# Kernel tuning notes

Hardware: AMD Instinct MI355X
Metric: run time of the kernel (lower is better)

## Reference

```python
import jax, jax.numpy as jnp
import numpy as np

GAMMA = 20
LAMBDA_INV = 25.0


def setup_inputs() -> dict:
    key = jax.random.key(0)
    k1, k2 = jax.random.split(key)
    B, P, D = 128, 512, 384
    z = jax.random.normal(k1, (B, P, D), dtype=jnp.float32)
    view_ids = jax.random.randint(k2, (P,), 0, 2, dtype=jnp.int64)
    return {"z": z, "view_ids": view_ids}


def reference(z, view_ids):
    B, P, D = z.shape
    # [B, P, P] pairwise similarity per image
    sim = jnp.einsum('bpd,bqd->bpq', z, z)
    # valid pairs: different view and not self
    mask_view = view_ids[None, :] != view_ids[:, None]          # [P, P]
    mask = mask_view & ~jnp.eye(P, dtype=bool)
    sim = jnp.where(mask[None, :, :], sim, jnp.float32(-1.0))
    best_sim = sim.max(axis=2)                                   # [B, P]
    best_j = sim.argmax(axis=2)                                  # [B, P]
    # flatten across batch, global top-gamma anchors
    best_sim_flat = best_sim.reshape(-1)                         # [B*P]
    offsets = jnp.arange(B, dtype=best_j.dtype)[:, None] * P
    best_j_flat = (best_j + offsets).reshape(-1)                 # [B*P]
    topk_vals, topk_idx = jax.lax.top_k(best_sim_flat, GAMMA)
    z_flat = z.reshape(-1, D)
    z1 = z_flat[topk_idx]                                        # anchors
    z2 = z_flat[best_j_flat[topk_idx]]                           # matches
    loss = LAMBDA_INV * jnp.mean((z1 - z2) ** 2)
    fmatch_avg_cos = jax.lax.stop_gradient(topk_vals.mean())
    return loss, fmatch_avg_cos
```

## Files before the change

kernel.cpp:

```cpp
#include <hip/hip_runtime.h>


#define NB 128
#define NP 512
#define ND 384
#define NGAMMA 20
#define NKS 12

typedef __attribute__((ext_vector_type(8))) short short8;
typedef __attribute__((ext_vector_type(4))) float f32x4;

__device__ __forceinline__ unsigned short f2bf(float f) {
    unsigned int u = __float_as_uint(f);
    u += 0x7fffu + ((u >> 16) & 1u);
    return (unsigned short)(u >> 16);
}

__device__ __forceinline__ void gload16(const void* gptr, void* lptr) {
    __builtin_amdgcn_global_load_lds(
        (const __attribute__((address_space(1))) void*)gptr,
        (__attribute__((address_space(3))) void*)lptr, 16, 0, 0);
}

__global__ __launch_bounds__(256) void fm_convert(
    const float* __restrict__ z, unsigned short* __restrict__ zt)
{
    __shared__ float ls[128][36];

    const int tid  = threadIdx.x;
    const int bid  = blockIdx.x;
    const int b    = bid / (NKS * 4);
    const int rem  = bid % (NKS * 4);
    const int kt   = rem >> 2;
    const int pblk = rem & 3;

    const float* zsrc = z + ((size_t)b * NP + pblk * 128) * ND + kt * 32;
#pragma unroll
    for (int i = 0; i < 4; ++i) {
        const int f   = tid + i * 256;
        const int row = f >> 3, c4 = f & 7;
        *(float4*)&ls[row][c4 * 4] = *(const float4*)(zsrc + (size_t)row * ND + c4 * 4);
    }
    __syncthreads();

    const int kg = tid >> 6, lane = tid & 63;
    unsigned short* dst = zt + (((size_t)b * NKS + kt) * 4 + kg) * 4096
                             + (size_t)pblk * 1024;
#pragma unroll
    for (int it = 0; it < 2; ++it) {
        const int row = it * 64 + lane;
        const float4 v0 = *(const float4*)&ls[row][kg * 8];
        const float4 v1 = *(const float4*)&ls[row][kg * 8 + 4];
        short8 s;
        s[0] = (short)f2bf(v0.x); s[1] = (short)f2bf(v0.y);
        s[2] = (short)f2bf(v0.z); s[3] = (short)f2bf(v0.w);
        s[4] = (short)f2bf(v1.x); s[5] = (short)f2bf(v1.y);
        s[6] = (short)f2bf(v1.z); s[7] = (short)f2bf(v1.w);
        *(short8*)(dst + (size_t)row * 8) = s;
    }
}

__global__ __launch_bounds__(512, 4) void fm_gemm(
    const unsigned short* __restrict__ zt, const int* __restrict__ view,
    float* __restrict__ pval, int* __restrict__ pidx)
{
    __shared__ __align__(16) unsigned short Ah[3][4][128][8];
    __shared__ __align__(16) unsigned short Bh[3][4][128][8];
    __shared__ int vs[NP];
    float* lsv = (float*)&Ah[0][0][0][0];
    int*   lsi = (int*)lsv + 512;
    float* lqv = (float*)lsv + 1024;
    int*   lqi = (int*)lsv + 1280;

    const int tid  = threadIdx.x;
    const int lane = tid & 63;
    const int wid  = tid >> 6;
    const int wr   = wid >> 2;
    const int wc2  = wid & 3;
    const int g    = lane >> 4, r = lane & 15;

    const int bid  = blockIdx.x;
    const int gidx = (bid & 7) * 160 + (bid >> 3);
    const int b    = gidx / 10;
    const int t    = gidx % 10;
    int tr, tc;
    if (t < 4)      { tr = 0; tc = t; }
    else if (t < 7) { tr = 1; tc = t - 3; }
    else if (t < 9) { tr = 2; tc = t - 5; }
    else            { tr = 3; tc = 3; }
    const bool diag = (tr == tc);
    const int p0 = tr * 128, q0 = tc * 128;

    vs[tid] = view[tid];
    __builtin_amdgcn_sched_barrier(0);

    f32x4 acc[4][2];
#pragma unroll
    for (int mi = 0; mi < 4; ++mi)
#pragma unroll
        for (int ni = 0; ni < 2; ++ni) acc[mi][ni] = (f32x4){0.f, 0.f, 0.f, 0.f};

#define STAGE(BUF, KT)                                                           \
    do {                                                                         \
        const int kg_ = wid >> 1;                                                \
        const int rb_ = (wid & 1) * 64;                                          \
        const size_t pl_ = (((size_t)b * NKS + (KT)) * 4 + kg_) * 4096;          \
        gload16(zt + pl_ + (size_t)(p0 + rb_ + lane) * 8, &Ah[BUF][kg_][rb_][0]); \
        gload16(zt + pl_ + (size_t)(q0 + rb_ + lane) * 8, &Bh[BUF][kg_][rb_][0]); \
    } while (0)

#define COMPUTE(BUF)                                                             \
    do {                                                                         \
        short8 ah_[4], bh_[2];                                                   \
        _Pragma("unroll")                                                        \
        for (int mi = 0; mi < 4; ++mi)                                           \
            ah_[mi] = *(const short8*)&Ah[BUF][g][wr * 64 + mi * 16 + r][0];     \
        _Pragma("unroll")                                                        \
        for (int ni = 0; ni < 2; ++ni)                                           \
            bh_[ni] = *(const short8*)&Bh[BUF][g][wc2 * 32 + ni * 16 + r][0];    \
        _Pragma("unroll")                                                        \
        for (int mi = 0; mi < 4; ++mi)                                           \
            _Pragma("unroll")                                                    \
            for (int ni = 0; ni < 2; ++ni)                                       \
                acc[mi][ni] = __builtin_amdgcn_mfma_f32_16x16x32_bf16(           \
                    ah_[mi], bh_[ni], acc[mi][ni], 0, 0, 0);                     \
    } while (0)

    STAGE(0, 0);
    STAGE(1, 1);
#pragma unroll
    for (int kt = 0; kt < NKS; ++kt) {
        if (kt < NKS - 1) asm volatile("s_waitcnt vmcnt(2)" ::: "memory");
        else              asm volatile("s_waitcnt vmcnt(0)" ::: "memory");
        __builtin_amdgcn_s_barrier();
        __builtin_amdgcn_sched_barrier(0);
        if (kt + 2 < NKS) STAGE((kt + 2) % 3, kt + 2);
        __builtin_amdgcn_sched_barrier(0);
        COMPUTE(kt % 3);
    }
#undef STAGE
#undef COMPUTE

#pragma unroll
    for (int mi = 0; mi < 4; ++mi) {
#pragma unroll
        for (int j = 0; j < 4; ++j) {
            const int prow = p0 + wr * 64 + mi * 16 + g * 4 + j;
            const int rv = vs[prow];
            float bv = -2.0f; int bq = 0;
#pragma unroll
            for (int ni = 0; ni < 2; ++ni) {
                const int q = q0 + wc2 * 32 + ni * 16 + r;
                const float v = (vs[q] != rv) ? acc[mi][ni][j] : -1.0f;
                if (v > bv) { bv = v; bq = q; }
            }
#pragma unroll
            for (int off = 1; off < 16; off <<= 1) {
                const float ov = __shfl_xor(bv, off);
                const int   oq = __shfl_xor(bq, off);
                if (ov > bv || (ov == bv && oq < bq)) { bv = ov; bq = oq; }
            }
            if (r == 0) {
                lsv[(wr * 4 + wc2) * 64 + mi * 16 + g * 4 + j] = bv;
                lsi[(wr * 4 + wc2) * 64 + mi * 16 + g * 4 + j] = bq;
            }
        }
    }
    if (!diag) {
#pragma unroll
        for (int ni = 0; ni < 2; ++ni) {
            const int q = q0 + wc2 * 32 + ni * 16 + r;
            const int qv = vs[q];
            float bv = -2.0f; int bp = 0;
#pragma unroll
            for (int mi = 0; mi < 4; ++mi)
#pragma unroll
                for (int j = 0; j < 4; ++j) {
                    const int prow = p0 + wr * 64 + mi * 16 + g * 4 + j;
                    const float v = (vs[prow] != qv) ? acc[mi][ni][j] : -1.0f;
                    if (v > bv) { bv = v; bp = prow; }
                }
#pragma unroll
            for (int off = 16; off < 64; off <<= 1) {
                const float ov = __shfl_xor(bv, off);
                const int   op = __shfl_xor(bp, off);
                if (ov > bv || (ov == bv && op < bp)) { bv = ov; bp = op; }
            }
            if (g == 0) {
                lqv[(wc2 * 2 + wr) * 32 + ni * 16 + r] = bv;
                lqi[(wc2 * 2 + wr) * 32 + ni * 16 + r] = bp;
            }
        }
    }
    __syncthreads();
    if (tid < 128) {
        {
            const int hw = tid >> 6, rw = tid & 63;
            float v0 = lsv[(hw * 4 + 0) * 64 + rw]; int i0 = lsi[(hw * 4 + 0) * 64 + rw];
#pragma unroll
            for (int c = 1; c < 4; ++c) {
                const float v1 = lsv[(hw * 4 + c) * 64 + rw];
                const int   i1 = lsi[(hw * 4 + c) * 64 + rw];
                if (v1 > v0) { v0 = v1; i0 = i1; }
            }
            pval[((size_t)b * NP + p0 + tid) * 4 + tc] = v0;
            pidx[((size_t)b * NP + p0 + tid) * 4 + tc] = i0;
        }
        if (!diag) {
            const int cg = tid >> 5, cw = tid & 31;
            float v0 = lqv[(cg * 2 + 0) * 32 + cw]; int i0 = lqi[(cg * 2 + 0) * 32 + cw];
            const float v1 = lqv[(cg * 2 + 1) * 32 + cw];
            const int   i1 = lqi[(cg * 2 + 1) * 32 + cw];
            if (v1 > v0) { v0 = v1; i0 = i1; }
            pval[((size_t)b * NP + q0 + tid) * 4 + tr] = v0;
            pidx[((size_t)b * NP + q0 + tid) * 4 + tr] = i0;
        }
    }
}

__global__ __launch_bounds__(64) void fm_topk_local(
    const float* __restrict__ pval, float* __restrict__ cval, int* __restrict__ cidx)
{
    const int lane = threadIdx.x;
    const int base = blockIdx.x * 1024;
    float v[16]; int id[16];
#pragma unroll
    for (int i = 0; i < 16; ++i) {
        const int a = base + i * 64 + lane;
        const float4 pv = ((const float4*)pval)[a];
        float bv = pv.x;
        if (pv.y > bv) bv = pv.y;
        if (pv.z > bv) bv = pv.z;
        if (pv.w > bv) bv = pv.w;
        v[i] = bv; id[i] = a;
    }
    for (int it = 0; it < NGAMMA; ++it) {
        float bv = v[0]; int bi = id[0];
#pragma unroll
        for (int i = 1; i < 16; ++i)
            if (v[i] > bv || (v[i] == bv && id[i] < bi)) { bv = v[i]; bi = id[i]; }
#pragma unroll
        for (int off = 1; off < 64; off <<= 1) {
            const float ov = __shfl_xor(bv, off);
            const int   oi = __shfl_xor(bi, off);
            if (ov > bv || (ov == bv && oi < bi)) { bv = ov; bi = oi; }
        }
        if (lane == 0) {
            cval[blockIdx.x * NGAMMA + it] = bv;
            cidx[blockIdx.x * NGAMMA + it] = bi;
        }
#pragma unroll
        for (int i = 0; i < 16; ++i) if (id[i] == bi) v[i] = -1e30f;
    }
}

__global__ __launch_bounds__(256) void fm_final(
    const float* __restrict__ cval, const int* __restrict__ cidx,
    const float* __restrict__ pval, const int* __restrict__ pidx,
    const float* __restrict__ z, float* __restrict__ out)
{
    __shared__ int sel[NGAMMA];
    __shared__ int selj[NGAMMA];
    __shared__ float red[4];

    const int t = threadIdx.x;
    const int lane = t & 63, w = t >> 6;
    float ssum = 0.f;

    if (w == 0) {
        float v[20]; int id[20];
#pragma unroll
        for (int i = 0; i < 20; ++i) {
            const int e = i * 64 + lane;
            v[i] = cval[e]; id[i] = cidx[e];
        }
        for (int it = 0; it < NGAMMA; ++it) {
            float bv = v[0]; int bi = id[0];
#pragma unroll
            for (int i = 1; i < 20; ++i)
                if (v[i] > bv || (v[i] == bv && id[i] < bi)) { bv = v[i]; bi = id[i]; }
#pragma unroll
            for (int off = 1; off < 64; off <<= 1) {
                const float ov = __shfl_xor(bv, off);
                const int   oi = __shfl_xor(bi, off);
                if (ov > bv || (ov == bv && oi < bi)) { bv = ov; bi = oi; }
            }
            if (lane == 0) sel[it] = bi;
            ssum += bv;
#pragma unroll
            for (int i = 0; i < 20; ++i) if (id[i] == bi) v[i] = -1e30f;
        }
        if (lane < NGAMMA) {
            const int a = sel[lane];
            const float4 pv = ((const float4*)pval)[a];
            float bv = pv.x; int bc = 0;
            if (pv.y > bv) { bv = pv.y; bc = 1; }
            if (pv.z > bv) { bv = pv.z; bc = 2; }
            if (pv.w > bv) { bv = pv.w; bc = 3; }
            selj[lane] = ((a >> 9) << 9) + pidx[(size_t)a * 4 + bc];
        }
    }
    __syncthreads();

    float acc = 0.f;
    for (int pr = 0; pr < NGAMMA; ++pr) {
        const int a = sel[pr];
        const int j = selj[pr];
        const float* za = z + (size_t)a * ND;
        const float* zj = z + (size_t)j * ND;
        for (int d = t; d < ND; d += 256) {
            const float df = za[d] - zj[d];
            acc = fmaf(df, df, acc);
        }
    }
#pragma unroll
    for (int off = 1; off < 64; off <<= 1) acc += __shfl_xor(acc, off);
    if (lane == 0) red[w] = acc;
    __syncthreads();
    if (t == 0) {
        const float tot = red[0] + red[1] + red[2] + red[3];
        out[0] = 25.0f * tot / (float)(NGAMMA * ND);
        out[1] = ssum / (float)NGAMMA;
    }
}

extern "C" void kernel_launch(void* const* d_in, const int* in_sizes, int n_in,
                              void* d_out, int out_size, void* d_ws, size_t ws_size,
                              hipStream_t stream)
{
    const float* z    = (const float*)d_in[0];
    const int*   view = (const int*)d_in[1];
    float*       out  = (float*)d_out;
    char* ws = (char*)d_ws;

    const size_t zt_off   = 0;
    const size_t pval_off = (size_t)NB * NP * ND * 2;
    const size_t pidx_off = pval_off + (size_t)NB * NP * 4 * 4;
    const size_t cval_off = pidx_off + (size_t)NB * NP * 4 * 4;
    const size_t cidx_off = cval_off + 64 * NGAMMA * 4;

    unsigned short* zt = (unsigned short*)(ws + zt_off);
    float* pval = (float*)(ws + pval_off);
    int*   pidx = (int*)(ws + pidx_off);
    float* cval = (float*)(ws + cval_off);
    int*   cidx = (int*)(ws + cidx_off);

    fm_convert<<<NB * NKS * 4, 256, 0, stream>>>(z, zt);
    fm_gemm<<<NB * 10, 512, 0, stream>>>(zt, view, pval, pidx);
    fm_topk_local<<<(NB * NP) / 1024, 64, 0, stream>>>(pval, cval, cidx);
    fm_final<<<1, 256, 0, stream>>>(cval, cidx, pval, pidx, z, out);
}
```

Measured before the change: 135.7 us.

## Reuse A tile for diagonal GEMM blocks and merge top-k tail into one kernel

On diagonal tiles the GEMM kernel skips loading the B operand, reads B fragments from the A shared-memory buffer, and adjusts the vmcnt wait count to match. The two tail kernels (per-block local top-k plus the final selection) are replaced by a single 1024-thread kernel. Each thread keeps its column's best candidate in shared memory, and only the winning thread rescans its column after a pick. This removes one launch and halves global loads on diagonal tiles, but the single-block tail has serial barrier-heavy iterations with little parallelism.

```diff
diff --git a/kernel.cpp b/kernel.cpp
--- a/kernel.cpp
+++ b/kernel.cpp
@@ -106,7 +106,8 @@
         const int rb_ = (wid & 1) * 64;                                          \
         const size_t pl_ = (((size_t)b * NKS + (KT)) * 4 + kg_) * 4096;          \
         gload16(zt + pl_ + (size_t)(p0 + rb_ + lane) * 8, &Ah[BUF][kg_][rb_][0]); \
-        gload16(zt + pl_ + (size_t)(q0 + rb_ + lane) * 8, &Bh[BUF][kg_][rb_][0]); \
+        if (!diag)                                                               \
+            gload16(zt + pl_ + (size_t)(q0 + rb_ + lane) * 8, &Bh[BUF][kg_][rb_][0]); \
     } while (0)
 
 #define COMPUTE(BUF)                                                             \
@@ -117,7 +118,8 @@
             ah_[mi] = *(const short8*)&Ah[BUF][g][wr * 64 + mi * 16 + r][0];     \
         _Pragma("unroll")                                                        \
         for (int ni = 0; ni < 2; ++ni)                                           \
-            bh_[ni] = *(const short8*)&Bh[BUF][g][wc2 * 32 + ni * 16 + r][0];    \
+            bh_[ni] = diag ? *(const short8*)&Ah[BUF][g][wc2 * 32 + ni * 16 + r][0] \
+                           : *(const short8*)&Bh[BUF][g][wc2 * 32 + ni * 16 + r][0]; \
         _Pragma("unroll")                                                        \
         for (int mi = 0; mi < 4; ++mi)                                           \
             _Pragma("unroll")                                                    \
@@ -130,8 +132,12 @@
     STAGE(1, 1);
 #pragma unroll
     for (int kt = 0; kt < NKS; ++kt) {
-        if (kt < NKS - 1) asm volatile("s_waitcnt vmcnt(2)" ::: "memory");
-        else              asm volatile("s_waitcnt vmcnt(0)" ::: "memory");
+        if (kt < NKS - 1) {
+            if (diag) asm volatile("s_waitcnt vmcnt(1)" ::: "memory");
+            else      asm volatile("s_waitcnt vmcnt(2)" ::: "memory");
+        } else {
+            asm volatile("s_waitcnt vmcnt(0)" ::: "memory");
+        }
         __builtin_amdgcn_s_barrier();
         __builtin_amdgcn_sched_barrier(0);
         if (kt + 2 < NKS) STAGE((kt + 2) % 3, kt + 2);
@@ -218,107 +224,105 @@
     }
 }
 
-__global__ __launch_bounds__(64) void fm_topk_local(
-    const float* __restrict__ pval, float* __restrict__ cval, int* __restrict__ cidx)
-{
-    const int lane = threadIdx.x;
-    const int base = blockIdx.x * 1024;
-    float v[16]; int id[16];
-#pragma unroll
-    for (int i = 0; i < 16; ++i) {
-        const int a = base + i * 64 + lane;
-        const float4 pv = ((const float4*)pval)[a];
-        float bv = pv.x;
-        if (pv.y > bv) bv = pv.y;
-        if (pv.z > bv) bv = pv.z;
-        if (pv.w > bv) bv = pv.w;
-        v[i] = bv; id[i] = a;
-    }
-    for (int it = 0; it < NGAMMA; ++it) {
-        float bv = v[0]; int bi = id[0];
-#pragma unroll
-        for (int i = 1; i < 16; ++i)
-            if (v[i] > bv || (v[i] == bv && id[i] < bi)) { bv = v[i]; bi = id[i]; }
-#pragma unroll
-        for (int off = 1; off < 64; off <<= 1) {
-            const float ov = __shfl_xor(bv, off);
-            const int   oi = __shfl_xor(bi, off);
-            if (ov > bv || (ov == bv && oi < bi)) { bv = ov; bi = oi; }
-        }
-        if (lane == 0) {
-            cval[blockIdx.x * NGAMMA + it] = bv;
-            cidx[blockIdx.x * NGAMMA + it] = bi;
-        }
-#pragma unroll
-        for (int i = 0; i < 16; ++i) if (id[i] == bi) v[i] = -1e30f;
-    }
-}
-
-__global__ __launch_bounds__(256) void fm_final(
-    const float* __restrict__ cval, const int* __restrict__ cidx,
+__global__ __launch_bounds__(1024) void fm_tail1(
     const float* __restrict__ pval, const int* __restrict__ pidx,
     const float* __restrict__ z, float* __restrict__ out)
 {
-    __shared__ int sel[NGAMMA];
-    __shared__ int selj[NGAMMA];
-    __shared__ float red[4];
+    __shared__ float cv[1024];
+    __shared__ int   ci[1024];
+    __shared__ float wv[16];
+    __shared__ int   wi[16];
+    __shared__ int   wo[16];
+    __shared__ int   wina, wino;
+    __shared__ int   sel[NGAMMA];
+    __shared__ int   selj[NGAMMA];
+    __shared__ float red[16];
 
     const int t = threadIdx.x;
     const int lane = t & 63, w = t >> 6;
+
+    unsigned long long mask = 0ULL;
+    {
+        float bv = -3.0f; int ba = 0;
+#pragma unroll
+        for (int i = 0; i < 64; ++i) {
+            const int a = i * 1024 + t;
+            const float4 pv = ((const float4*)pval)[a];
+            float v = pv.x;
+            if (pv.y > v) v = pv.y;
+            if (pv.z > v) v = pv.z;
+            if (pv.w > v) v = pv.w;
+            if (v > bv) { bv = v; ba = a; }
+        }
+        cv[t] = bv; ci[t] = ba;
+    }
+    __syncthreads();
+
     float ssum = 0.f;
-
-    if (w == 0) {
-        float v[20]; int id[20];
-#pragma unroll
-        for (int i = 0; i < 20; ++i) {
-            const int e = i * 64 + lane;
-            v[i] = cval[e]; id[i] = cidx[e];
-        }
-        for (int it = 0; it < NGAMMA; ++it) {
-            float bv = v[0]; int bi = id[0];
-#pragma unroll
-            for (int i = 1; i < 20; ++i)
-                if (v[i] > bv || (v[i] == bv && id[i] < bi)) { bv = v[i]; bi = id[i]; }
-#pragma unroll
-            for (int off = 1; off < 64; off <<= 1) {
-                const float ov = __shfl_xor(bv, off);
-                const int   oi = __shfl_xor(bi, off);
-                if (ov > bv || (ov == bv && oi < bi)) { bv = ov; bi = oi; }
-            }
-            if (lane == 0) sel[it] = bi;
-            ssum += bv;
-#pragma unroll
-            for (int i = 0; i < 20; ++i) if (id[i] == bi) v[i] = -1e30f;
-        }
-        if (lane < NGAMMA) {
-            const int a = sel[lane];
-            const float4 pv = ((const float4*)pval)[a];
-            float bv = pv.x; int bc = 0;
-            if (pv.y > bv) { bv = pv.y; bc = 1; }
-            if (pv.z > bv) { bv = pv.z; bc = 2; }
-            if (pv.w > bv) { bv = pv.w; bc = 3; }
-            selj[lane] = ((a >> 9) << 9) + pidx[(size_t)a * 4 + bc];
-        }
+    for (int it = 0; it < NGAMMA; ++it) {
+        float v = cv[t]; int a = ci[t]; int own = t;
+#pragma unroll
+        for (int off = 1; off < 64; off <<= 1) {
+            const float ov = __shfl_xor(v, off);
+            const int   oa = __shfl_xor(a, off);
+            const int   oo = __shfl_xor(own, off);
+            if (ov > v || (ov == v && oa < a)) { v = ov; a = oa; own = oo; }
+        }
+        if (lane == 0) { wv[w] = v; wi[w] = a; wo[w] = own; }
+        __syncthreads();
+        if (t == 0) {
+            float bv2 = wv[0]; int ba2 = wi[0], bo2 = wo[0];
+            for (int k = 1; k < 16; ++k)
+                if (wv[k] > bv2 || (wv[k] == bv2 && wi[k] < ba2)) {
+                    bv2 = wv[k]; ba2 = wi[k]; bo2 = wo[k];
+                }
+            wina = ba2; wino = bo2;
+            sel[it] = ba2;
+            ssum += bv2;
+        }
+        __syncthreads();
+        if (t == wino) {
+            mask |= 1ULL << (unsigned)(wina >> 10);
+            float nb = -3.0f; int na = 0;
+            for (int i = 0; i < 64; ++i) {
+                if ((mask >> i) & 1ULL) continue;
+                const int aa = i * 1024 + t;
+                const float4 pv = ((const float4*)pval)[aa];
+                float vv = pv.x;
+                if (pv.y > vv) vv = pv.y;
+                if (pv.z > vv) vv = pv.z;
+                if (pv.w > vv) vv = pv.w;
+                if (vv > nb) { nb = vv; na = aa; }
+            }
+            cv[t] = nb; ci[t] = na;
+        }
+        __syncthreads();
+    }
+
+    if (t < NGAMMA) {
+        const int a = sel[t];
+        const float4 pv = ((const float4*)pval)[a];
+        float bv = pv.x; int bc = 0;
+        if (pv.y > bv) { bv = pv.y; bc = 1; }
+        if (pv.z > bv) { bv = pv.z; bc = 2; }
+        if (pv.w > bv) { bv = pv.w; bc = 3; }
+        selj[t] = ((a >> 9) << 9) + pidx[(size_t)a * 4 + bc];
     }
     __syncthreads();
 
     float acc = 0.f;
-    for (int pr = 0; pr < NGAMMA; ++pr) {
-        const int a = sel[pr];
-        const int j = selj[pr];
-        const float* za = z + (size_t)a * ND;
-        const float* zj = z + (size_t)j * ND;
-        for (int d = t; d < ND; d += 256) {
-            const float df = za[d] - zj[d];
-            acc = fmaf(df, df, acc);
-        }
+    for (int e = t; e < NGAMMA * ND; e += 1024) {
+        const int pr = e / ND, d = e - pr * ND;
+        const float df = z[(size_t)sel[pr] * ND + d] - z[(size_t)selj[pr] * ND + d];
+        acc = fmaf(df, df, acc);
     }
 #pragma unroll
     for (int off = 1; off < 64; off <<= 1) acc += __shfl_xor(acc, off);
     if (lane == 0) red[w] = acc;
     __syncthreads();
     if (t == 0) {
-        const float tot = red[0] + red[1] + red[2] + red[3];
+        float tot = 0.f;
+        for (int k = 0; k < 16; ++k) tot += red[k];
         out[0] = 25.0f * tot / (float)(NGAMMA * ND);
         out[1] = ssum / (float)NGAMMA;
     }
@@ -336,17 +340,12 @@
     const size_t zt_off   = 0;
     const size_t pval_off = (size_t)NB * NP * ND * 2;
     const size_t pidx_off = pval_off + (size_t)NB * NP * 4 * 4;
-    const size_t cval_off = pidx_off + (size_t)NB * NP * 4 * 4;
-    const size_t cidx_off = cval_off + 64 * NGAMMA * 4;
 
     unsigned short* zt = (unsigned short*)(ws + zt_off);
     float* pval = (float*)(ws + pval_off);
     int*   pidx = (int*)(ws + pidx_off);
-    float* cval = (float*)(ws + cval_off);
-    int*   cidx = (int*)(ws + cidx_off);
 
     fm_convert<<<NB * NKS * 4, 256, 0, stream>>>(z, zt);
     fm_gemm<<<NB * 10, 512, 0, stream>>>(zt, view, pval, pidx);
-    fm_topk_local<<<(NB * NP) / 1024, 64, 0, stream>>>(pval, cval, cidx);
-    fm_final<<<1, 256, 0, stream>>>(cval, cidx, pval, pidx, z, out);
-}
+    fm_tail1<<<1, 1024, 0, stream>>>(pval, pidx, z, out);
+}
```

Result: slower. 322.0 us (+137.3%).
